# Performance work log

Measured on AMD Instinct MI355X. Metric: run time of the kernel, lower is better.

The kernel has to match this reference:

```python
import jax, jax.numpy as jnp
import numpy as np

N_NODES = 100000
N_EDGES = 1600000
N_CLASS = 45


def gcn_conv(x, W, b, src, dst, ew, n):
    # PyG GCNConv: add self-loops (weight 1), symmetric deg^-1/2 normalization,
    # linear transform, scatter-add aggregation into targets, then bias.
    loops = jnp.arange(n, dtype=src.dtype)
    s = jnp.concatenate([src, loops])
    d = jnp.concatenate([dst, loops])
    w = jnp.concatenate([ew, jnp.ones((n,), ew.dtype)])
    deg = jax.ops.segment_sum(w, d, num_segments=n)          # in-degree (weighted)
    dis = jnp.where(deg > 0, 1.0 / jnp.sqrt(deg), 0.0)      # deg^-1/2, 0 where deg==0
    norm = dis[s] * w * dis[d]                               # [E+n]
    h = x @ W                                                # [n, out]
    out = jax.ops.segment_sum(h[s] * norm[:, None], d, num_segments=n)
    return out + b


def setup_inputs() -> dict:
    key = jax.random.key(0)
    ks = jax.random.split(key, 6)
    x = jax.random.normal(ks[0], (N_NODES, N_CLASS), dtype=jnp.float32)
    edge_src = jax.random.randint(ks[1], (N_EDGES,), 0, N_NODES, dtype=jnp.int64 if jax.config.jax_enable_x64 else jnp.int32).astype(jnp.int32)
    edge_dst = jax.random.randint(ks[2], (N_EDGES,), 0, N_NODES, dtype=jnp.int64 if jax.config.jax_enable_x64 else jnp.int32).astype(jnp.int32)
    edge_w = jax.random.uniform(ks[3], (N_EDGES,), dtype=jnp.float32)
    W1 = jax.random.normal(ks[4], (N_CLASS, 32), dtype=jnp.float32) / np.sqrt(N_CLASS)
    b1 = jnp.zeros((32,), dtype=jnp.float32)
    W2 = jax.random.normal(ks[5], (32, 128), dtype=jnp.float32) / np.sqrt(32.0)
    b2 = jnp.zeros((128,), dtype=jnp.float32)
    return {"x": x, "edge_src": edge_src, "edge_dst": edge_dst, "edge_w": edge_w,
            "W1": W1, "b1": b1, "W2": W2, "b2": b2}


def reference(x, edge_src, edge_dst, edge_w, W1, b1, W2, b2):
    n = x.shape[0]
    h = jnp.tanh(gcn_conv(x, W1, b1, edge_src, edge_dst, edge_w, n))
    return gcn_conv(h, W2, b2, edge_src, edge_dst, edge_w, n)
```

## Files before the change

kernel.cpp:

```cpp
#include <hip/hip_runtime.h>
#include <hip/hip_fp16.h>
#include <math.h>

static constexpr int TPB = 256;
static constexpr int NPB_SHIFT = 8;
static constexpr int BCAP = 5120;
static constexpr int PCHUNK = 4096;

__device__ __forceinline__ int p_src(unsigned p) { return (int)(p >> 15); }
__device__ __forceinline__ float p_w(unsigned p) {
  return __half2float(__ushort_as_half((unsigned short)(p & 0x7FFFu)));
}

__global__ void k_zero(int* __restrict__ bkcnt, int NB) {
  int i = blockIdx.x * blockDim.x + threadIdx.x;
  if (i < NB) bkcnt[i] = 0;
}

__global__ void k_partition(const int* __restrict__ src, const int* __restrict__ dst,
                            const float* __restrict__ ew, int* __restrict__ bkcnt,
                            unsigned* __restrict__ ppk, unsigned char* __restrict__ pld,
                            int E, int NB) {
  __shared__ int lh[512];
  __shared__ int lbase[512];
  __shared__ int lcur[512];
  int tid = threadIdx.x;
  long long e0 = (long long)blockIdx.x * PCHUNK;
  int d[PCHUNK / TPB];
  unsigned pk[PCHUNK / TPB];
  for (int t = tid; t < NB; t += TPB) { lh[t] = 0; lcur[t] = 0; }
  __syncthreads();
#pragma unroll
  for (int r = 0; r < PCHUNK / TPB; ++r) {
    long long e = e0 + (long long)r * TPB + tid;
    if (e < E) {
      d[r] = dst[e];
      pk[r] = ((unsigned)src[e] << 15) |
              ((unsigned)__half_as_ushort(__float2half(ew[e])) & 0x7FFFu);
      atomicAdd(&lh[d[r] >> NPB_SHIFT], 1);
    } else {
      d[r] = -1;
    }
  }
  __syncthreads();
  for (int t = tid; t < NB; t += TPB)
    lbase[t] = lh[t] ? (t * BCAP + atomicAdd(&bkcnt[t], lh[t])) : 0;
  __syncthreads();
#pragma unroll
  for (int r = 0; r < PCHUNK / TPB; ++r) {
    if (d[r] >= 0) {
      int b = d[r] >> NPB_SHIFT;
      int pos = atomicAdd(&lcur[b], 1);
      size_t gp = (size_t)lbase[b] + pos;
      ppk[gp] = pk[r];
      pld[gp] = (unsigned char)(d[r] & 255);
    }
  }
}

__global__ void __launch_bounds__(TPB) k_bucket(const unsigned* __restrict__ ppk,
                                                const unsigned char* __restrict__ pld,
                                                const int* __restrict__ bkcnt,
                                                unsigned* __restrict__ csr,
                                                int2* __restrict__ rc,
                                                float* __restrict__ dis,
                                                const float* __restrict__ x,
                                                const float* __restrict__ W1,
                                                __half2* __restrict__ hh, int n) {
  __shared__ unsigned lpk[BCAP];
  __shared__ unsigned char lld[BCAP];
  __shared__ float sW[45 * 32];
  __shared__ int lcnt[256];
  __shared__ int lofs[256];
  __shared__ float lsum[256];
  int b = blockIdx.x;
  int t = threadIdx.x;
  int beg = b * BCAP;
  int m = bkcnt[b];
  if (m > BCAP) m = BCAP;
  lcnt[t] = 0;
  lsum[t] = 0.f;
  for (int i = t; i < 45 * 32; i += TPB) sW[i] = W1[i];
  __syncthreads();
  for (int i = t; i < m; i += TPB) {
    unsigned pk = ppk[(size_t)beg + i];
    unsigned char ld = pld[(size_t)beg + i];
    lpk[i] = pk;
    lld[i] = ld;
    atomicAdd(&lcnt[ld], 1);
  }
  __syncthreads();
  int v = lcnt[t];
  lofs[t] = v;
  __syncthreads();
  for (int off = 1; off < 256; off <<= 1) {
    int tv = (t >= off) ? lofs[t - off] : 0;
    __syncthreads();
    lofs[t] += tv;
    __syncthreads();
  }
  int ex = lofs[t] - v;
  int gnode = (b << NPB_SHIFT) + t;
  if (gnode < n) rc[gnode] = make_int2(beg + ex, v);
  lcnt[t] = ex;
  __syncthreads();
  for (int i = t; i < m; i += TPB) {
    unsigned pk = lpk[i];
    int ld = lld[i];
    int pos = atomicAdd(&lcnt[ld], 1);
    csr[(size_t)beg + pos] = pk;
    atomicAdd(&lsum[ld], p_w(pk));
  }
  __syncthreads();
  if (gnode < n) {
    float dsc = rsqrtf(1.0f + lsum[t]);
    dis[gnode] = dsc;
    float xr[45];
#pragma unroll
    for (int k = 0; k < 45; ++k) xr[k] = x[(size_t)gnode * 45 + k];
    __half2* hw = hh + (size_t)gnode * 16;
#pragma unroll 2
    for (int j2 = 0; j2 < 16; ++j2) {
      float a0 = 0.f, a1 = 0.f;
#pragma unroll
      for (int k = 0; k < 45; ++k) {
        a0 = fmaf(xr[k], sW[k * 32 + j2 * 2], a0);
        a1 = fmaf(xr[k], sW[k * 32 + j2 * 2 + 1], a1);
      }
      hw[j2] = __floats2half2_rn(a0 * dsc, a1 * dsc);
    }
  }
}

template <bool TANH>
__global__ void k_gather(const unsigned* __restrict__ csr, const int2* __restrict__ rc,
                         const float* __restrict__ dis, const __half2* __restrict__ hh,
                         const float* __restrict__ b1, __half2* __restrict__ outv, int n) {
  int gid = blockIdx.x * blockDim.x + threadIdx.x;
  int wave = gid >> 6;
  int lane = threadIdx.x & 63;
  int g = lane >> 4;
  int j2 = lane & 15;
  int node = wave * 2 + (g >> 1);
  int strm = g & 1;
  if (node >= n) return;
  int2 r = rc[node];
  const unsigned* row = csr + r.x;
  int m = r.y;
  float ax0 = 0.f, ay0 = 0.f, ax1 = 0.f, ay1 = 0.f;
  float ax2 = 0.f, ay2 = 0.f, ax3 = 0.f, ay3 = 0.f;
  int e = strm;
  for (; e + 6 < m; e += 8) {
    unsigned p0 = row[e], p1 = row[e + 2], p2 = row[e + 4], p3 = row[e + 6];
    float2 v0 = __half22float2(hh[(size_t)p_src(p0) * 16 + j2]);
    float2 v1 = __half22float2(hh[(size_t)p_src(p1) * 16 + j2]);
    float2 v2 = __half22float2(hh[(size_t)p_src(p2) * 16 + j2]);
    float2 v3 = __half22float2(hh[(size_t)p_src(p3) * 16 + j2]);
    float w0 = p_w(p0), w1 = p_w(p1), w2 = p_w(p2), w3 = p_w(p3);
    ax0 = fmaf(w0, v0.x, ax0); ay0 = fmaf(w0, v0.y, ay0);
    ax1 = fmaf(w1, v1.x, ax1); ay1 = fmaf(w1, v1.y, ay1);
    ax2 = fmaf(w2, v2.x, ax2); ay2 = fmaf(w2, v2.y, ay2);
    ax3 = fmaf(w3, v3.x, ax3); ay3 = fmaf(w3, v3.y, ay3);
  }
  if (e + 2 < m) {
    unsigned p0 = row[e], p1 = row[e + 2];
    float2 v0 = __half22float2(hh[(size_t)p_src(p0) * 16 + j2]);
    float2 v1 = __half22float2(hh[(size_t)p_src(p1) * 16 + j2]);
    float w0 = p_w(p0), w1 = p_w(p1);
    ax0 = fmaf(w0, v0.x, ax0); ay0 = fmaf(w0, v0.y, ay0);
    ax1 = fmaf(w1, v1.x, ax1); ay1 = fmaf(w1, v1.y, ay1);
    e += 4;
  }
  if (e < m) {
    unsigned p = row[e];
    float2 v = __half22float2(hh[(size_t)p_src(p) * 16 + j2]);
    float w = p_w(p);
    ax0 = fmaf(w, v.x, ax0); ay0 = fmaf(w, v.y, ay0);
  }
  float ax = (ax0 + ax1) + (ax2 + ax3);
  float ay = (ay0 + ay1) + (ay2 + ay3);
  ax += __shfl_xor(ax, 16, 64);
  ay += __shfl_xor(ay, 16, 64);
  if (strm == 0) {
    float dd = dis[node];
    float2 own = __half22float2(hh[(size_t)node * 16 + j2]);
    if (TANH) {
      float2 bv = reinterpret_cast<const float2*>(b1)[j2];
      float r0 = bv.x + dd * (ax + own.x);
      float r1 = bv.y + dd * (ay + own.y);
      outv[(size_t)node * 16 + j2] = __floats2half2_rn(dd * tanhf(r0), dd * tanhf(r1));
    } else {
      outv[(size_t)node * 16 + j2] = __floats2half2_rn(dd * (ax + own.x), dd * (ay + own.y));
    }
  }
}

__global__ void k_gemm2(const __half2* __restrict__ y, const float* __restrict__ W2,
                        const float* __restrict__ b2, float* __restrict__ out, int n) {
  __shared__ float sW[32 * 128];
  __shared__ float sB[128];
  for (int t = threadIdx.x; t < 32 * 128; t += blockDim.x) sW[t] = W2[t];
  if (threadIdx.x < 128) sB[threadIdx.x] = b2[threadIdx.x];
  __syncthreads();
  int gid = blockIdx.x * blockDim.x + threadIdx.x;
  int node = gid >> 2;
  if (node >= n) return;
  int g4 = (gid & 3) * 4;
  float4 a[8];
#pragma unroll
  for (int q = 0; q < 8; ++q) a[q] = *reinterpret_cast<const float4*>(&sB[g4 + q * 16]);
  const __half2* yr = y + (size_t)node * 16;
#pragma unroll
  for (int k2 = 0; k2 < 16; ++k2) {
    float2 yv = __half22float2(yr[k2]);
    const float* w0 = &sW[(k2 * 2) * 128 + g4];
    const float* w1 = &sW[(k2 * 2 + 1) * 128 + g4];
#pragma unroll
    for (int q = 0; q < 8; ++q) {
      float4 wa = *reinterpret_cast<const float4*>(w0 + q * 16);
      float4 wb = *reinterpret_cast<const float4*>(w1 + q * 16);
      a[q].x = fmaf(yv.x, wa.x, fmaf(yv.y, wb.x, a[q].x));
      a[q].y = fmaf(yv.x, wa.y, fmaf(yv.y, wb.y, a[q].y));
      a[q].z = fmaf(yv.x, wa.z, fmaf(yv.y, wb.z, a[q].z));
      a[q].w = fmaf(yv.x, wa.w, fmaf(yv.y, wb.w, a[q].w));
    }
  }
  float* op = out + (size_t)node * 128 + g4;
#pragma unroll
  for (int q = 0; q < 8; ++q) *reinterpret_cast<float4*>(op + q * 16) = a[q];
}

static inline dim3 gx(long long work) { return dim3((unsigned)((work + TPB - 1) / TPB)); }

extern "C" void kernel_launch(void* const* d_in, const int* in_sizes, int n_in,
                              void* d_out, int out_size, void* d_ws, size_t ws_size,
                              hipStream_t stream) {
  const float* x   = (const float*)d_in[0];
  const int*   src = (const int*)d_in[1];
  const int*   dst = (const int*)d_in[2];
  const float* ew  = (const float*)d_in[3];
  const float* W1  = (const float*)d_in[4];
  const float* b1  = (const float*)d_in[5];
  const float* W2  = (const float*)d_in[6];
  const float* b2  = (const float*)d_in[7];
  float* out = (float*)d_out;

  const int n = in_sizes[0] / 45;
  const int E = in_sizes[1];
  const int NB = (n + 255) >> NPB_SHIFT;

  char* w = (char*)d_ws;
  size_t o = 0;
  auto alloc = [&](size_t bytes) { void* p = w + o; o += ((bytes + 255) & ~(size_t)255); return p; };
  int*           bkcnt = (int*)          alloc((size_t)NB * 4);
  unsigned*      ppk   = (unsigned*)     alloc((size_t)NB * BCAP * 4);
  unsigned char* pld   = (unsigned char*)alloc((size_t)NB * BCAP);
  unsigned*      csr   = (unsigned*)     alloc((size_t)NB * BCAP * 4);
  int2*          rc    = (int2*)         alloc((size_t)n * 8);
  float*         dis   = (float*)        alloc((size_t)n * 4);
  __half2*       hh    = (__half2*)      alloc((size_t)n * 32 * 2);
  __half2*       ag1   = (__half2*)      alloc((size_t)n * 32 * 2);
  __half2*       y     = (__half2*)      alloc((size_t)n * 32 * 2);

  const int PB = (E + PCHUNK - 1) / PCHUNK;

  k_zero<<<gx(NB), TPB, 0, stream>>>(bkcnt, NB);
  k_partition<<<PB, TPB, 0, stream>>>(src, dst, ew, bkcnt, ppk, pld, E, NB);
  k_bucket<<<NB, TPB, 0, stream>>>(ppk, pld, bkcnt, csr, rc, dis, x, W1, hh, n);
  k_gather<true><<<gx((long long)n * 32), TPB, 0, stream>>>(csr, rc, dis, hh, b1, ag1, n);
  k_gather<false><<<gx((long long)n * 32), TPB, 0, stream>>>(csr, rc, dis, ag1, b1, y, n);
  k_gemm2<<<gx((long long)n * 4), TPB, 0, stream>>>(y, W2, b2, out, n);
}
```

Baseline: 151.8 us.

## Remap gather to 4 threads per node with 16-byte vector loads

The gather kernel now assigns 4 threads per node, each loading 16 bytes (4 half2) per neighbor row, instead of 32 threads per node split into two edge streams, each loading one half2. This cuts the thread count 8x and replaces narrow per-lane loads with wider vector loads. It also drops the cross-lane shuffle reduction. Each thread now walks the whole neighbor list serially, so latency per node grows and load balance depends more on degree variance. The zeroing kernel is also replaced by hipMemsetAsync.

Result: faster. 141.7 us (-6.7%).

```diff
diff --git a/kernel.cpp b/kernel.cpp
--- a/kernel.cpp
+++ b/kernel.cpp
@@ -12,10 +12,7 @@
   return __half2float(__ushort_as_half((unsigned short)(p & 0x7FFFu)));
 }
 
-__global__ void k_zero(int* __restrict__ bkcnt, int NB) {
-  int i = blockIdx.x * blockDim.x + threadIdx.x;
-  if (i < NB) bkcnt[i] = 0;
-}
+struct h2x4 { __half2 a, b, c, d; };
 
 __global__ void k_partition(const int* __restrict__ src, const int* __restrict__ dst,
                             const float* __restrict__ ew, int* __restrict__ bkcnt,
@@ -137,61 +134,74 @@
                          const float* __restrict__ dis, const __half2* __restrict__ hh,
                          const float* __restrict__ b1, __half2* __restrict__ outv, int n) {
   int gid = blockIdx.x * blockDim.x + threadIdx.x;
-  int wave = gid >> 6;
-  int lane = threadIdx.x & 63;
-  int g = lane >> 4;
-  int j2 = lane & 15;
-  int node = wave * 2 + (g >> 1);
-  int strm = g & 1;
+  int node = gid >> 2;
   if (node >= n) return;
+  int q = (threadIdx.x & 3) * 4;
   int2 r = rc[node];
   const unsigned* row = csr + r.x;
   int m = r.y;
-  float ax0 = 0.f, ay0 = 0.f, ax1 = 0.f, ay1 = 0.f;
-  float ax2 = 0.f, ay2 = 0.f, ax3 = 0.f, ay3 = 0.f;
-  int e = strm;
-  for (; e + 6 < m; e += 8) {
-    unsigned p0 = row[e], p1 = row[e + 2], p2 = row[e + 4], p3 = row[e + 6];
-    float2 v0 = __half22float2(hh[(size_t)p_src(p0) * 16 + j2]);
-    float2 v1 = __half22float2(hh[(size_t)p_src(p1) * 16 + j2]);
-    float2 v2 = __half22float2(hh[(size_t)p_src(p2) * 16 + j2]);
-    float2 v3 = __half22float2(hh[(size_t)p_src(p3) * 16 + j2]);
+  const __half2* tbl = hh + q;
+  float2 c0 = {0.f, 0.f}, c1 = {0.f, 0.f}, c2 = {0.f, 0.f}, c3 = {0.f, 0.f};
+  float2 d0 = {0.f, 0.f}, d1 = {0.f, 0.f}, d2 = {0.f, 0.f}, d3 = {0.f, 0.f};
+  int e = 0;
+  for (; e + 3 < m; e += 4) {
+    unsigned p0 = row[e], p1 = row[e + 1], p2 = row[e + 2], p3 = row[e + 3];
+    h2x4 v0 = *reinterpret_cast<const h2x4*>(tbl + (size_t)p_src(p0) * 16);
+    h2x4 v1 = *reinterpret_cast<const h2x4*>(tbl + (size_t)p_src(p1) * 16);
+    h2x4 v2 = *reinterpret_cast<const h2x4*>(tbl + (size_t)p_src(p2) * 16);
+    h2x4 v3 = *reinterpret_cast<const h2x4*>(tbl + (size_t)p_src(p3) * 16);
     float w0 = p_w(p0), w1 = p_w(p1), w2 = p_w(p2), w3 = p_w(p3);
-    ax0 = fmaf(w0, v0.x, ax0); ay0 = fmaf(w0, v0.y, ay0);
-    ax1 = fmaf(w1, v1.x, ax1); ay1 = fmaf(w1, v1.y, ay1);
-    ax2 = fmaf(w2, v2.x, ax2); ay2 = fmaf(w2, v2.y, ay2);
-    ax3 = fmaf(w3, v3.x, ax3); ay3 = fmaf(w3, v3.y, ay3);
-  }
-  if (e + 2 < m) {
-    unsigned p0 = row[e], p1 = row[e + 2];
-    float2 v0 = __half22float2(hh[(size_t)p_src(p0) * 16 + j2]);
-    float2 v1 = __half22float2(hh[(size_t)p_src(p1) * 16 + j2]);
-    float w0 = p_w(p0), w1 = p_w(p1);
-    ax0 = fmaf(w0, v0.x, ax0); ay0 = fmaf(w0, v0.y, ay0);
-    ax1 = fmaf(w1, v1.x, ax1); ay1 = fmaf(w1, v1.y, ay1);
-    e += 4;
-  }
-  if (e < m) {
+    float2 f;
+    f = __half22float2(v0.a); c0.x = fmaf(w0, f.x, c0.x); c0.y = fmaf(w0, f.y, c0.y);
+    f = __half22float2(v0.b); c1.x = fmaf(w0, f.x, c1.x); c1.y = fmaf(w0, f.y, c1.y);
+    f = __half22float2(v0.c); c2.x = fmaf(w0, f.x, c2.x); c2.y = fmaf(w0, f.y, c2.y);
+    f = __half22float2(v0.d); c3.x = fmaf(w0, f.x, c3.x); c3.y = fmaf(w0, f.y, c3.y);
+    f = __half22float2(v1.a); d0.x = fmaf(w1, f.x, d0.x); d0.y = fmaf(w1, f.y, d0.y);
+    f = __half22float2(v1.b); d1.x = fmaf(w1, f.x, d1.x); d1.y = fmaf(w1, f.y, d1.y);
+    f = __half22float2(v1.c); d2.x = fmaf(w1, f.x, d2.x); d2.y = fmaf(w1, f.y, d2.y);
+    f = __half22float2(v1.d); d3.x = fmaf(w1, f.x, d3.x); d3.y = fmaf(w1, f.y, d3.y);
+    f = __half22float2(v2.a); c0.x = fmaf(w2, f.x, c0.x); c0.y = fmaf(w2, f.y, c0.y);
+    f = __half22float2(v2.b); c1.x = fmaf(w2, f.x, c1.x); c1.y = fmaf(w2, f.y, c1.y);
+    f = __half22float2(v2.c); c2.x = fmaf(w2, f.x, c2.x); c2.y = fmaf(w2, f.y, c2.y);
+    f = __half22float2(v2.d); c3.x = fmaf(w2, f.x, c3.x); c3.y = fmaf(w2, f.y, c3.y);
+    f = __half22float2(v3.a); d0.x = fmaf(w3, f.x, d0.x); d0.y = fmaf(w3, f.y, d0.y);
+    f = __half22float2(v3.b); d1.x = fmaf(w3, f.x, d1.x); d1.y = fmaf(w3, f.y, d1.y);
+    f = __half22float2(v3.c); d2.x = fmaf(w3, f.x, d2.x); d2.y = fmaf(w3, f.y, d2.y);
+    f = __half22float2(v3.d); d3.x = fmaf(w3, f.x, d3.x); d3.y = fmaf(w3, f.y, d3.y);
+  }
+  for (; e < m; ++e) {
     unsigned p = row[e];
-    float2 v = __half22float2(hh[(size_t)p_src(p) * 16 + j2]);
+    h2x4 v = *reinterpret_cast<const h2x4*>(tbl + (size_t)p_src(p) * 16);
     float w = p_w(p);
-    ax0 = fmaf(w, v.x, ax0); ay0 = fmaf(w, v.y, ay0);
-  }
-  float ax = (ax0 + ax1) + (ax2 + ax3);
-  float ay = (ay0 + ay1) + (ay2 + ay3);
-  ax += __shfl_xor(ax, 16, 64);
-  ay += __shfl_xor(ay, 16, 64);
-  if (strm == 0) {
-    float dd = dis[node];
-    float2 own = __half22float2(hh[(size_t)node * 16 + j2]);
-    if (TANH) {
-      float2 bv = reinterpret_cast<const float2*>(b1)[j2];
-      float r0 = bv.x + dd * (ax + own.x);
-      float r1 = bv.y + dd * (ay + own.y);
-      outv[(size_t)node * 16 + j2] = __floats2half2_rn(dd * tanhf(r0), dd * tanhf(r1));
-    } else {
-      outv[(size_t)node * 16 + j2] = __floats2half2_rn(dd * (ax + own.x), dd * (ay + own.y));
-    }
+    float2 f;
+    f = __half22float2(v.a); c0.x = fmaf(w, f.x, c0.x); c0.y = fmaf(w, f.y, c0.y);
+    f = __half22float2(v.b); c1.x = fmaf(w, f.x, c1.x); c1.y = fmaf(w, f.y, c1.y);
+    f = __half22float2(v.c); c2.x = fmaf(w, f.x, c2.x); c2.y = fmaf(w, f.y, c2.y);
+    f = __half22float2(v.d); c3.x = fmaf(w, f.x, c3.x); c3.y = fmaf(w, f.y, c3.y);
+  }
+  c0.x += d0.x; c0.y += d0.y; c1.x += d1.x; c1.y += d1.y;
+  c2.x += d2.x; c2.y += d2.y; c3.x += d3.x; c3.y += d3.y;
+  float dd = dis[node];
+  h2x4 own = *reinterpret_cast<const h2x4*>(hh + (size_t)node * 16 + q);
+  __half2* op = outv + (size_t)node * 16 + q;
+  float2 o0 = __half22float2(own.a), o1 = __half22float2(own.b);
+  float2 o2 = __half22float2(own.c), o3 = __half22float2(own.d);
+  if (TANH) {
+    const float4* bp = reinterpret_cast<const float4*>(b1 + q * 2);
+    float4 ba = bp[0], bb = bp[1];
+    op[0] = __floats2half2_rn(dd * tanhf(ba.x + dd * (c0.x + o0.x)),
+                              dd * tanhf(ba.y + dd * (c0.y + o0.y)));
+    op[1] = __floats2half2_rn(dd * tanhf(ba.z + dd * (c1.x + o1.x)),
+                              dd * tanhf(ba.w + dd * (c1.y + o1.y)));
+    op[2] = __floats2half2_rn(dd * tanhf(bb.x + dd * (c2.x + o2.x)),
+                              dd * tanhf(bb.y + dd * (c2.y + o2.y)));
+    op[3] = __floats2half2_rn(dd * tanhf(bb.z + dd * (c3.x + o3.x)),
+                              dd * tanhf(bb.w + dd * (c3.y + o3.y)));
+  } else {
+    op[0] = __floats2half2_rn(dd * (c0.x + o0.x), dd * (c0.y + o0.y));
+    op[1] = __floats2half2_rn(dd * (c1.x + o1.x), dd * (c1.y + o1.y));
+    op[2] = __floats2half2_rn(dd * (c2.x + o2.x), dd * (c2.y + o2.y));
+    op[3] = __floats2half2_rn(dd * (c3.x + o3.x), dd * (c3.y + o3.y));
   }
 }
 
@@ -264,10 +274,10 @@
 
   const int PB = (E + PCHUNK - 1) / PCHUNK;
 
-  k_zero<<<gx(NB), TPB, 0, stream>>>(bkcnt, NB);
+  hipMemsetAsync(bkcnt, 0, (size_t)NB * 4, stream);
   k_partition<<<PB, TPB, 0, stream>>>(src, dst, ew, bkcnt, ppk, pld, E, NB);
   k_bucket<<<NB, TPB, 0, stream>>>(ppk, pld, bkcnt, csr, rc, dis, x, W1, hh, n);
-  k_gather<true><<<gx((long long)n * 32), TPB, 0, stream>>>(csr, rc, dis, hh, b1, ag1, n);
-  k_gather<false><<<gx((long long)n * 32), TPB, 0, stream>>>(csr, rc, dis, ag1, b1, y, n);
+  k_gather<true><<<gx((long long)n * 4), TPB, 0, stream>>>(csr, rc, dis, hh, b1, ag1, n);
+  k_gather<false><<<gx((long long)n * 4), TPB, 0, stream>>>(csr, rc, dis, ag1, b1, y, n);
   k_gemm2<<<gx((long long)n * 4), TPB, 0, stream>>>(y, W2, b2, out, n);
 }
```
